# Kernel optimization log

Hardware: AMD Instinct MI355X
Metric: run time of the kernel (lower is better)

## Reference

```python
import jax, jax.numpy as jnp
import numpy as np

K = 3  # from init kwarg


def setup_inputs() -> dict:
    key = jax.random.key(0)
    k1, k2 = jax.random.split(key)
    B, N, D = 32, 2048, 128
    features = jax.random.normal(k1, (B, N, D), dtype=jnp.float32)
    strength = jax.random.uniform(k2, (), dtype=jnp.float32)
    return {"features": features, "strength": strength}


def reference(features, strength):
    B, N, D = features.shape
    k = min(K, N - 1)
    x = jax.lax.stop_gradient(features)  # torch uses features.detach() for the mix path

    # pairwise euclidean distance (torch.cdist, p=2): ||a||^2 + ||b||^2 - 2 a.b
    sq = jnp.sum(x * x, axis=-1)                     # (B, N)
    d2 = sq[:, :, None] + sq[:, None, :] - 2.0 * jnp.einsum('bnd,bmd->bnm', x, x)
    dist = jnp.sqrt(jnp.maximum(d2, 0.0))            # (B, N, N)

    # mask self-distance with +1e6 on the diagonal
    eye = jnp.eye(N, dtype=dist.dtype)
    dist = dist + eye[None, :, :] * 1000000.0

    # k smallest -> top_k of negated distances
    _, idx = jax.lax.top_k(-dist, k)                 # idx: (B, N, k)

    # gather neighbor features: gathered[b,n,j] = x[b, idx[b,n,j]]
    gathered = x[jnp.arange(B)[:, None, None], idx]  # (B, N, k, D)
    mix = jnp.mean(gathered, axis=2)                 # (B, N, D)

    s = jnp.clip(strength, 0.0, 1.0)
    return (1.0 - s) * features + s * mix
```

## Files before the change

kernel.cpp:

```cpp
#include <hip/hip_runtime.h>
#include <cfloat>

#define BB 32
#define NN 2048
#define DD 128
#define RM 128
#define CN 64

typedef __attribute__((ext_vector_type(8))) short short8;
typedef __attribute__((ext_vector_type(4))) float float4v;

__device__ __forceinline__ unsigned short f2bf(float f) {
    unsigned int u = __builtin_bit_cast(unsigned int, f);
    u += 0x7FFFu + ((u >> 16) & 1u);
    return (unsigned short)(u >> 16);
}

__device__ __forceinline__ unsigned int umn(unsigned int a, unsigned int b) { return a < b ? a : b; }
__device__ __forceinline__ unsigned int umx(unsigned int a, unsigned int b) { return a > b ? a : b; }
#define CSU(a, b) { unsigned int _lo = umn(a, b), _hi = umx(a, b); (a) = _lo; (b) = _hi; }

__device__ __forceinline__ void gl2lds16(const unsigned short* g, unsigned short* l) {
    __builtin_amdgcn_global_load_lds(
        (const __attribute__((address_space(1))) void*)g,
        (__attribute__((address_space(3))) void*)l, 16, 0, 0);
}

__global__ __launch_bounds__(256) void prep_kernel(const float* __restrict__ x,
        unsigned short* __restrict__ xb16, float* __restrict__ sq) {
    int t = blockIdx.x * 256 + threadIdx.x;
    int row = t >> 2;
    int q = t & 3;
    const float4* xp = reinterpret_cast<const float4*>(x + (size_t)row * DD + q * 32);
    unsigned short* op = xb16 + (size_t)row * DD + q * 32;
    float acc = 0.f;
#pragma unroll
    for (int i = 0; i < 4; ++i) {
        float4 v0 = xp[2 * i], v1 = xp[2 * i + 1];
        acc += v0.x * v0.x + v0.y * v0.y + v0.z * v0.z + v0.w * v0.w;
        acc += v1.x * v1.x + v1.y * v1.y + v1.z * v1.z + v1.w * v1.w;
        short8 pk;
        pk[0] = (short)f2bf(v0.x); pk[1] = (short)f2bf(v0.y);
        pk[2] = (short)f2bf(v0.z); pk[3] = (short)f2bf(v0.w);
        pk[4] = (short)f2bf(v1.x); pk[5] = (short)f2bf(v1.y);
        pk[6] = (short)f2bf(v1.z); pk[7] = (short)f2bf(v1.w);
        *reinterpret_cast<short8*>(op + i * 8) = pk;
    }
    acc += __shfl_xor(acc, 1);
    acc += __shfl_xor(acc, 2);
    if (q == 0) sq[row] = acc;
}

__global__ __launch_bounds__(256) void sq_kernel(const float* __restrict__ x,
                                                 float* __restrict__ sq) {
    int t = blockIdx.x * 256 + threadIdx.x;
    int row = t >> 2;
    int q = t & 3;
    const float4* xp = reinterpret_cast<const float4*>(x + (size_t)row * DD + q * 32);
    float acc = 0.f;
#pragma unroll
    for (int i = 0; i < 8; ++i) {
        float4 v = xp[i];
        acc += v.x * v.x + v.y * v.y + v.z * v.z + v.w * v.w;
    }
    acc += __shfl_xor(acc, 1);
    acc += __shfl_xor(acc, 2);
    if (q == 0) sq[row] = acc;
}

template<bool PRE>
__global__ __launch_bounds__(256, 2) void knn_kernel(const float* __restrict__ x,
        const unsigned short* __restrict__ xb16g,
        const float* __restrict__ sqv, const float* __restrict__ strength,
        float* __restrict__ out) {
    __shared__ __align__(16) unsigned short btile[2 * CN * DD];
    __shared__ unsigned int cand8[RM * 8];

    const int b = blockIdx.x;
    const int row0 = blockIdx.y * RM;
    const int tid = threadIdx.x;
    const int w = tid >> 6;
    const int lane = tid & 63;
    const int m = lane & 15;
    const int quad = lane >> 4;
    const float* __restrict__ xb = x + (size_t)b * NN * DD;
    const unsigned short* __restrict__ gb = PRE ? xb16g + (size_t)b * NN * DD : nullptr;

    short8 afrag[2][4];
    if constexpr (PRE) {
#pragma unroll
        for (int rg = 0; rg < 2; ++rg)
#pragma unroll
            for (int kc = 0; kc < 4; ++kc)
                afrag[rg][kc] = *reinterpret_cast<const short8*>(
                    gb + (size_t)(row0 + 32 * w + rg * 16 + m) * DD + kc * 32 + quad * 8);
    } else {
#pragma unroll
        for (int rg = 0; rg < 2; ++rg)
#pragma unroll
            for (int kc = 0; kc < 4; ++kc) {
                const float4* src = reinterpret_cast<const float4*>(
                    xb + (size_t)(row0 + 32 * w + rg * 16 + m) * DD + kc * 32 + quad * 8);
                float4 v0 = src[0], v1 = src[1];
                short8 pk;
                pk[0] = (short)f2bf(v0.x); pk[1] = (short)f2bf(v0.y);
                pk[2] = (short)f2bf(v0.z); pk[3] = (short)f2bf(v0.w);
                pk[4] = (short)f2bf(v1.x); pk[5] = (short)f2bf(v1.y);
                pk[6] = (short)f2bf(v1.z); pk[7] = (short)f2bf(v1.w);
                afrag[rg][kc] = pk;
            }
    }

    {
        unsigned short* buf = btile;
        if constexpr (PRE) {
#pragma unroll
            for (int l = 0; l < 4; ++l) {
                int f = (l * 4 + w) * 64 + lane;
                int r = f >> 4, p = f & 15;
                int c = p ^ (r & 7);
                gl2lds16(gb + (size_t)r * DD + c * 8, buf + (l * 4 + w) * 512);
            }
        } else {
#pragma unroll
            for (int l = 0; l < 4; ++l) {
                int id = l * 256 + tid;
                int r = id >> 4, c = id & 15, p = c ^ (r & 7);
                const float4* src = reinterpret_cast<const float4*>(xb + (size_t)r * DD + c * 8);
                float4 v0 = src[0], v1 = src[1];
                short8 pk;
                pk[0] = (short)f2bf(v0.x); pk[1] = (short)f2bf(v0.y);
                pk[2] = (short)f2bf(v0.z); pk[3] = (short)f2bf(v0.w);
                pk[4] = (short)f2bf(v1.x); pk[5] = (short)f2bf(v1.y);
                pk[6] = (short)f2bf(v1.z); pk[7] = (short)f2bf(v1.w);
                *reinterpret_cast<short8*>(buf + r * DD + p * 8) = pk;
            }
        }
    }
    __syncthreads();

    unsigned int tk[2][4][4];
#pragma unroll
    for (int rg = 0; rg < 2; ++rg)
#pragma unroll
        for (int i = 0; i < 4; ++i)
#pragma unroll
            for (int q = 0; q < 4; ++q) tk[rg][i][q] = 0xFFFFFFFFu;

    for (int ct = 0; ct < NN / CN; ++ct) {
        unsigned short* cur = btile + (size_t)(ct & 1) * CN * DD;
        unsigned short* nxt = btile + (size_t)((ct + 1) & 1) * CN * DD;

        if (ct + 1 < NN / CN) {
            int cb = (ct + 1) * CN;
            if constexpr (PRE) {
#pragma unroll
                for (int l = 0; l < 4; ++l) {
                    int f = (l * 4 + w) * 64 + lane;
                    int r = f >> 4, p = f & 15;
                    int c = p ^ (r & 7);
                    gl2lds16(gb + (size_t)(cb + r) * DD + c * 8, nxt + (l * 4 + w) * 512);
                }
            } else {
#pragma unroll
                for (int l = 0; l < 4; ++l) {
                    int id = l * 256 + tid;
                    int r = id >> 4, c = id & 15, p = c ^ (r & 7);
                    const float4* src = reinterpret_cast<const float4*>(xb + (size_t)(cb + r) * DD + c * 8);
                    float4 v0 = src[0], v1 = src[1];
                    short8 pk;
                    pk[0] = (short)f2bf(v0.x); pk[1] = (short)f2bf(v0.y);
                    pk[2] = (short)f2bf(v0.z); pk[3] = (short)f2bf(v0.w);
                    pk[4] = (short)f2bf(v1.x); pk[5] = (short)f2bf(v1.y);
                    pk[6] = (short)f2bf(v1.z); pk[7] = (short)f2bf(v1.w);
                    *reinterpret_cast<short8*>(nxt + r * DD + p * 8) = pk;
                }
            }
        }

        float sqb[4];
#pragma unroll
        for (int cc = 0; cc < 4; ++cc)
            sqb[cc] = sqv[(size_t)b * NN + ct * CN + cc * 16 + m] + 1024.0f;

        float4v acc[2][4];
#pragma unroll
        for (int rg = 0; rg < 2; ++rg)
#pragma unroll
            for (int cc = 0; cc < 4; ++cc) acc[rg][cc] = (float4v){0.f, 0.f, 0.f, 0.f};
#pragma unroll
        for (int kc = 0; kc < 4; ++kc) {
            short8 bfrag[4];
#pragma unroll
            for (int cc = 0; cc < 4; ++cc) {
                int rl = cc * 16 + m;
                int p = (kc * 4 + quad) ^ (m & 7);
                bfrag[cc] = *reinterpret_cast<const short8*>(cur + rl * DD + p * 8);
            }
#pragma unroll
            for (int rg = 0; rg < 2; ++rg)
#pragma unroll
                for (int cc = 0; cc < 4; ++cc)
                    acc[rg][cc] = __builtin_amdgcn_mfma_f32_16x16x32_bf16(
                        afrag[rg][kc], bfrag[cc], acc[rg][cc], 0, 0, 0);
        }

#pragma unroll
        for (int cc = 0; cc < 4; ++cc) {
            unsigned int col = (unsigned int)(ct * CN + cc * 16 + m);
#pragma unroll
            for (int rg = 0; rg < 2; ++rg)
#pragma unroll
                for (int reg = 0; reg < 4; ++reg) {
                    float scb = fmaf(-2.f, acc[rg][cc][reg], sqb[cc]);
                    unsigned int key = (__builtin_bit_cast(unsigned int, scb) & 0xFFFFF800u) | col;
                    unsigned int n;
                    n = umn(tk[rg][reg][0], key); key = umx(tk[rg][reg][0], key); tk[rg][reg][0] = n;
                    n = umn(tk[rg][reg][1], key); key = umx(tk[rg][reg][1], key); tk[rg][reg][1] = n;
                    n = umn(tk[rg][reg][2], key); key = umx(tk[rg][reg][2], key); tk[rg][reg][2] = n;
                    tk[rg][reg][3] = umn(tk[rg][reg][3], key);
                }
        }

        __syncthreads();
    }

#pragma unroll
    for (int rg = 0; rg < 2; ++rg)
#pragma unroll
        for (int reg = 0; reg < 4; ++reg) {
            unsigned int e[8];
#pragma unroll
            for (int j = 0; j < 4; ++j) e[j] = tk[rg][reg][j];
#pragma unroll
            for (int j = 4; j < 8; ++j) e[j] = 0xFFFFFFFFu;
#pragma unroll
            for (int st = 0; st < 4; ++st) {
                int mask = 1 << st;
                unsigned int rv[8];
#pragma unroll
                for (int j = 0; j < 8; ++j)
                    rv[j] = (unsigned int)__shfl_xor((int)e[7 - j], mask, 64);
#pragma unroll
                for (int j = 0; j < 8; ++j) e[j] = umn(e[j], rv[j]);
                CSU(e[0], e[4]); CSU(e[1], e[5]); CSU(e[2], e[6]); CSU(e[3], e[7]);
                CSU(e[0], e[2]); CSU(e[1], e[3]); CSU(e[4], e[6]); CSU(e[5], e[7]);
                CSU(e[0], e[1]); CSU(e[2], e[3]); CSU(e[4], e[5]); CSU(e[6], e[7]);
            }
            if (m == 0) {
                int row = 32 * w + rg * 16 + quad * 4 + reg;
#pragma unroll
                for (int j = 0; j < 8; ++j) cand8[row * 8 + j] = e[j];
            }
        }
    __syncthreads();

    double* refd = reinterpret_cast<double*>(btile);
    int* best3 = reinterpret_cast<int*>(btile) + 2048;

    {
        int r = tid >> 1, h = tid & 1;
        int grow = row0 + r;
        int ci[4];
#pragma unroll
        for (int j = 0; j < 4; ++j) ci[j] = (int)(cand8[r * 8 + h * 4 + j] & 0x7FFu);
        const float* pr = xb + (size_t)grow * DD;
        const float* pc[4];
#pragma unroll
        for (int j = 0; j < 4; ++j) pc[j] = xb + (size_t)ci[j] * DD;
        double a[4] = {0.0, 0.0, 0.0, 0.0};
#pragma unroll 4
        for (int d4 = 0; d4 < 32; ++d4) {
            float4 wv = *reinterpret_cast<const float4*>(pr + d4 * 4);
#pragma unroll
            for (int j = 0; j < 4; ++j) {
                float4 v = *reinterpret_cast<const float4*>(pc[j] + d4 * 4);
                double d;
                d = (double)wv.x - (double)v.x; a[j] += d * d;
                d = (double)wv.y - (double)v.y; a[j] += d * d;
                d = (double)wv.z - (double)v.z; a[j] += d * d;
                d = (double)wv.w - (double)v.w; a[j] += d * d;
            }
        }
#pragma unroll
        for (int j = 0; j < 4; ++j)
            refd[r * 8 + h * 4 + j] = (ci[j] == grow) ? DBL_MAX : a[j];
    }
    __syncthreads();

    if (tid < RM) {
        int r = tid;
        double b0 = DBL_MAX, b1 = DBL_MAX, b2 = DBL_MAX;
        int i0 = 0x7fffffff, i1 = 0x7fffffff, i2 = 0x7fffffff;
        for (int e = 0; e < 8; ++e) {
            double dv = refd[r * 8 + e];
            int ix = (int)(cand8[r * 8 + e] & 0x7FFu);
            if (dv < b2 || (dv == b2 && ix < i2)) {
                b2 = dv; i2 = ix;
                if (b1 > b2 || (b1 == b2 && i1 > i2)) { double td = b1; b1 = b2; b2 = td; int tn = i1; i1 = i2; i2 = tn; }
                if (b0 > b1 || (b0 == b1 && i0 > i1)) { double td = b0; b0 = b1; b1 = td; int tn = i0; i0 = i1; i1 = tn; }
            }
        }
        best3[r * 3 + 0] = i0; best3[r * 3 + 1] = i1; best3[r * 3 + 2] = i2;
    }
    __syncthreads();

    {
        int r = tid >> 1, q = tid & 1;
        float s = fminf(fmaxf(strength[0], 0.f), 1.f);
        const float* pa = xb + (size_t)(row0 + r) * DD + q * 64;
        const float* p1 = xb + (size_t)best3[r * 3 + 0] * DD + q * 64;
        const float* p2 = xb + (size_t)best3[r * 3 + 1] * DD + q * 64;
        const float* p3 = xb + (size_t)best3[r * 3 + 2] * DD + q * 64;
        float* po = out + ((size_t)b * NN + row0 + r) * DD + q * 64;
#pragma unroll
        for (int l = 0; l < 16; ++l) {
            float4 a  = *reinterpret_cast<const float4*>(pa + l * 4);
            float4 n1 = *reinterpret_cast<const float4*>(p1 + l * 4);
            float4 n2 = *reinterpret_cast<const float4*>(p2 + l * 4);
            float4 n3 = *reinterpret_cast<const float4*>(p3 + l * 4);
            float4 o;
            o.x = (1.f - s) * a.x + s * ((n1.x + n2.x + n3.x) / 3.f);
            o.y = (1.f - s) * a.y + s * ((n1.y + n2.y + n3.y) / 3.f);
            o.z = (1.f - s) * a.z + s * ((n1.z + n2.z + n3.z) / 3.f);
            o.w = (1.f - s) * a.w + s * ((n1.w + n2.w + n3.w) / 3.f);
            *reinterpret_cast<float4*>(po + l * 4) = o;
        }
    }
}

extern "C" void kernel_launch(void* const* d_in, const int* in_sizes, int n_in,
                              void* d_out, int out_size, void* d_ws, size_t ws_size,
                              hipStream_t stream) {
    const float* x = (const float*)d_in[0];
    const float* strength = (const float*)d_in[1];
    float* out = (float*)d_out;
    float* sq = (float*)d_ws;
    unsigned short* xb16 = (unsigned short*)((char*)d_ws + 256 * 1024);
    const size_t need = 256 * 1024 + (size_t)BB * NN * DD * sizeof(unsigned short);

    if (ws_size >= need) {
        prep_kernel<<<dim3((BB * NN * 4) / 256), 256, 0, stream>>>(x, xb16, sq);
        knn_kernel<true><<<dim3(BB, NN / RM), 256, 0, stream>>>(x, xb16, sq, strength, out);
    } else {
        sq_kernel<<<dim3((BB * NN * 4) / 256), 256, 0, stream>>>(x, sq);
        knn_kernel<false><<<dim3(BB, NN / RM), 256, 0, stream>>>(x, nullptr, sq, strength, out);
    }
}
```

Baseline: 200.8 us.

## Split kNN column range across blocks and move refinement into separate finish kernel

The main kNN kernel now splits the candidate column range into halves along a third grid dimension, doubling the block count. Each block writes its per-row top-8 approximate candidates to workspace. A new finish kernel recomputes exact double-precision distances for the merged candidates, picks the best three and performs the blend. The aim is more parallelism and occupancy (launch bounds raised to 4 blocks per CU) in exchange for an extra launch and a global round-trip of candidate keys. The last fallback path writes candidates without checking that the workspace is large enough.

```diff
diff --git a/kernel.cpp b/kernel.cpp
--- a/kernel.cpp
+++ b/kernel.cpp
@@ -69,15 +69,18 @@
 }
 
 template<bool PRE>
-__global__ __launch_bounds__(256, 2) void knn_kernel(const float* __restrict__ x,
+__global__ __launch_bounds__(256, 4) void knn_main(const float* __restrict__ x,
         const unsigned short* __restrict__ xb16g,
-        const float* __restrict__ sqv, const float* __restrict__ strength,
-        float* __restrict__ out) {
+        const float* __restrict__ sqv,
+        unsigned int* __restrict__ top8, int halves) {
     __shared__ __align__(16) unsigned short btile[2 * CN * DD];
-    __shared__ unsigned int cand8[RM * 8];
 
     const int b = blockIdx.x;
     const int row0 = blockIdx.y * RM;
+    const int h = blockIdx.z;
+    const int colspan = NN / halves;
+    const int col0 = h * colspan;
+    const int tiles = colspan / CN;
     const int tid = threadIdx.x;
     const int w = tid >> 6;
     const int lane = tid & 63;
@@ -119,14 +122,14 @@
                 int f = (l * 4 + w) * 64 + lane;
                 int r = f >> 4, p = f & 15;
                 int c = p ^ (r & 7);
-                gl2lds16(gb + (size_t)r * DD + c * 8, buf + (l * 4 + w) * 512);
+                gl2lds16(gb + (size_t)(col0 + r) * DD + c * 8, buf + (l * 4 + w) * 512);
             }
         } else {
 #pragma unroll
             for (int l = 0; l < 4; ++l) {
                 int id = l * 256 + tid;
                 int r = id >> 4, c = id & 15, p = c ^ (r & 7);
-                const float4* src = reinterpret_cast<const float4*>(xb + (size_t)r * DD + c * 8);
+                const float4* src = reinterpret_cast<const float4*>(xb + (size_t)(col0 + r) * DD + c * 8);
                 float4 v0 = src[0], v1 = src[1];
                 short8 pk;
                 pk[0] = (short)f2bf(v0.x); pk[1] = (short)f2bf(v0.y);
@@ -147,12 +150,13 @@
 #pragma unroll
             for (int q = 0; q < 4; ++q) tk[rg][i][q] = 0xFFFFFFFFu;
 
-    for (int ct = 0; ct < NN / CN; ++ct) {
+    for (int ct = 0; ct < tiles; ++ct) {
         unsigned short* cur = btile + (size_t)(ct & 1) * CN * DD;
         unsigned short* nxt = btile + (size_t)((ct + 1) & 1) * CN * DD;
-
-        if (ct + 1 < NN / CN) {
-            int cb = (ct + 1) * CN;
+        int colbase = col0 + ct * CN;
+
+        if (ct + 1 < tiles) {
+            int cb = colbase + CN;
             if constexpr (PRE) {
 #pragma unroll
                 for (int l = 0; l < 4; ++l) {
@@ -181,7 +185,7 @@
         float sqb[4];
 #pragma unroll
         for (int cc = 0; cc < 4; ++cc)
-            sqb[cc] = sqv[(size_t)b * NN + ct * CN + cc * 16 + m] + 1024.0f;
+            sqb[cc] = sqv[(size_t)b * NN + colbase + cc * 16 + m] + 1024.0f;
 
         float4v acc[2][4];
 #pragma unroll
@@ -207,7 +211,7 @@
 
 #pragma unroll
         for (int cc = 0; cc < 4; ++cc) {
-            unsigned int col = (unsigned int)(ct * CN + cc * 16 + m);
+            unsigned int col = (unsigned int)(colbase + cc * 16 + m);
 #pragma unroll
             for (int rg = 0; rg < 2; ++rg)
 #pragma unroll
@@ -248,73 +252,80 @@
                 CSU(e[0], e[1]); CSU(e[2], e[3]); CSU(e[4], e[5]); CSU(e[6], e[7]);
             }
             if (m == 0) {
-                int row = 32 * w + rg * 16 + quad * 4 + reg;
-#pragma unroll
-                for (int j = 0; j < 8; ++j) cand8[row * 8 + j] = e[j];
-            }
-        }
-    __syncthreads();
-
-    double* refd = reinterpret_cast<double*>(btile);
-    int* best3 = reinterpret_cast<int*>(btile) + 2048;
-
-    {
-        int r = tid >> 1, h = tid & 1;
-        int grow = row0 + r;
-        int ci[4];
-#pragma unroll
-        for (int j = 0; j < 4; ++j) ci[j] = (int)(cand8[r * 8 + h * 4 + j] & 0x7FFu);
-        const float* pr = xb + (size_t)grow * DD;
-        const float* pc[4];
-#pragma unroll
-        for (int j = 0; j < 4; ++j) pc[j] = xb + (size_t)ci[j] * DD;
-        double a[4] = {0.0, 0.0, 0.0, 0.0};
+                int row = row0 + 32 * w + rg * 16 + quad * 4 + reg;
+                unsigned int* dst = top8 + ((size_t)(b * NN + row) * halves + h) * 8;
+#pragma unroll
+                for (int j = 0; j < 8; ++j) dst[j] = e[j];
+            }
+        }
+}
+
+__global__ __launch_bounds__(256) void finish_kernel(const float* __restrict__ x,
+        const unsigned int* __restrict__ top8, const float* __restrict__ strength,
+        float* __restrict__ out, int halves) {
+    __shared__ double refd[32 * 16];
+    __shared__ int cidx[32 * 16];
+    __shared__ int best3[32 * 3];
+
+    const int tid = threadIdx.x;
+    const int r = tid >> 3;
+    const int t8 = tid & 7;
+    const int R = blockIdx.x * 32 + r;
+    const int b = R >> 11;
+    const int n = R & (NN - 1);
+    const float* __restrict__ xb = x + (size_t)b * NN * DD;
+    const int ncand = 8 * halves;
+
+    const unsigned int* keys = top8 + (size_t)R * ncand;
+    const int npt = halves;
+#pragma unroll 2
+    for (int t = 0; t < npt; ++t) {
+        int j = t8 * npt + t;
+        int ix = (int)(keys[j] & 0x7FFu);
+        const float* pc = xb + (size_t)ix * DD;
+        const float* pr = xb + (size_t)n * DD;
+        double a = 0.0;
 #pragma unroll 4
         for (int d4 = 0; d4 < 32; ++d4) {
             float4 wv = *reinterpret_cast<const float4*>(pr + d4 * 4);
-#pragma unroll
-            for (int j = 0; j < 4; ++j) {
-                float4 v = *reinterpret_cast<const float4*>(pc[j] + d4 * 4);
-                double d;
-                d = (double)wv.x - (double)v.x; a[j] += d * d;
-                d = (double)wv.y - (double)v.y; a[j] += d * d;
-                d = (double)wv.z - (double)v.z; a[j] += d * d;
-                d = (double)wv.w - (double)v.w; a[j] += d * d;
-            }
-        }
-#pragma unroll
-        for (int j = 0; j < 4; ++j)
-            refd[r * 8 + h * 4 + j] = (ci[j] == grow) ? DBL_MAX : a[j];
+            float4 v = *reinterpret_cast<const float4*>(pc + d4 * 4);
+            double d;
+            d = (double)wv.x - (double)v.x; a += d * d;
+            d = (double)wv.y - (double)v.y; a += d * d;
+            d = (double)wv.z - (double)v.z; a += d * d;
+            d = (double)wv.w - (double)v.w; a += d * d;
+        }
+        refd[r * 16 + j] = (ix == n) ? DBL_MAX : a;
+        cidx[r * 16 + j] = ix;
     }
     __syncthreads();
 
-    if (tid < RM) {
-        int r = tid;
+    if (tid < 32) {
+        int rr = tid;
         double b0 = DBL_MAX, b1 = DBL_MAX, b2 = DBL_MAX;
         int i0 = 0x7fffffff, i1 = 0x7fffffff, i2 = 0x7fffffff;
-        for (int e = 0; e < 8; ++e) {
-            double dv = refd[r * 8 + e];
-            int ix = (int)(cand8[r * 8 + e] & 0x7FFu);
+        for (int e = 0; e < ncand; ++e) {
+            double dv = refd[rr * 16 + e];
+            int ix = cidx[rr * 16 + e];
             if (dv < b2 || (dv == b2 && ix < i2)) {
                 b2 = dv; i2 = ix;
                 if (b1 > b2 || (b1 == b2 && i1 > i2)) { double td = b1; b1 = b2; b2 = td; int tn = i1; i1 = i2; i2 = tn; }
                 if (b0 > b1 || (b0 == b1 && i0 > i1)) { double td = b0; b0 = b1; b1 = td; int tn = i0; i0 = i1; i1 = tn; }
             }
         }
-        best3[r * 3 + 0] = i0; best3[r * 3 + 1] = i1; best3[r * 3 + 2] = i2;
+        best3[rr * 3 + 0] = i0; best3[rr * 3 + 1] = i1; best3[rr * 3 + 2] = i2;
     }
     __syncthreads();
 
     {
-        int r = tid >> 1, q = tid & 1;
         float s = fminf(fmaxf(strength[0], 0.f), 1.f);
-        const float* pa = xb + (size_t)(row0 + r) * DD + q * 64;
-        const float* p1 = xb + (size_t)best3[r * 3 + 0] * DD + q * 64;
-        const float* p2 = xb + (size_t)best3[r * 3 + 1] * DD + q * 64;
-        const float* p3 = xb + (size_t)best3[r * 3 + 2] * DD + q * 64;
-        float* po = out + ((size_t)b * NN + row0 + r) * DD + q * 64;
-#pragma unroll
-        for (int l = 0; l < 16; ++l) {
+        const float* pa = xb + (size_t)n * DD + t8 * 16;
+        const float* p1 = xb + (size_t)best3[r * 3 + 0] * DD + t8 * 16;
+        const float* p2 = xb + (size_t)best3[r * 3 + 1] * DD + t8 * 16;
+        const float* p3 = xb + (size_t)best3[r * 3 + 2] * DD + t8 * 16;
+        float* po = out + (size_t)R * DD + t8 * 16;
+#pragma unroll
+        for (int l = 0; l < 4; ++l) {
             float4 a  = *reinterpret_cast<const float4*>(pa + l * 4);
             float4 n1 = *reinterpret_cast<const float4*>(p1 + l * 4);
             float4 n2 = *reinterpret_cast<const float4*>(p2 + l * 4);
@@ -335,15 +346,36 @@
     const float* x = (const float*)d_in[0];
     const float* strength = (const float*)d_in[1];
     float* out = (float*)d_out;
+
+    const size_t SQ_B = 256 * 1024;
+    const size_t BF_B = (size_t)BB * NN * DD * 2;
     float* sq = (float*)d_ws;
-    unsigned short* xb16 = (unsigned short*)((char*)d_ws + 256 * 1024);
-    const size_t need = 256 * 1024 + (size_t)BB * NN * DD * sizeof(unsigned short);
-
-    if (ws_size >= need) {
+
+    const size_t need_pre2 = SQ_B + BF_B + (size_t)BB * NN * 2 * 8 * 4;
+    const size_t need_pre1 = SQ_B + BF_B + (size_t)BB * NN * 1 * 8 * 4;
+    const size_t need_raw2 = SQ_B + (size_t)BB * NN * 2 * 8 * 4;
+
+    if (ws_size >= need_pre2) {
+        unsigned short* xb16 = (unsigned short*)((char*)d_ws + SQ_B);
+        unsigned int* top8 = (unsigned int*)((char*)d_ws + SQ_B + BF_B);
         prep_kernel<<<dim3((BB * NN * 4) / 256), 256, 0, stream>>>(x, xb16, sq);
-        knn_kernel<true><<<dim3(BB, NN / RM), 256, 0, stream>>>(x, xb16, sq, strength, out);
+        knn_main<true><<<dim3(BB, NN / RM, 2), 256, 0, stream>>>(x, xb16, sq, top8, 2);
+        finish_kernel<<<dim3(BB * NN / 32), 256, 0, stream>>>(x, top8, strength, out, 2);
+    } else if (ws_size >= need_pre1) {
+        unsigned short* xb16 = (unsigned short*)((char*)d_ws + SQ_B);
+        unsigned int* top8 = (unsigned int*)((char*)d_ws + SQ_B + BF_B);
+        prep_kernel<<<dim3((BB * NN * 4) / 256), 256, 0, stream>>>(x, xb16, sq);
+        knn_main<true><<<dim3(BB, NN / RM, 1), 256, 0, stream>>>(x, xb16, sq, top8, 1);
+        finish_kernel<<<dim3(BB * NN / 32), 256, 0, stream>>>(x, top8, strength, out, 1);
+    } else if (ws_size >= need_raw2) {
+        unsigned int* top8 = (unsigned int*)((char*)d_ws + SQ_B);
+        sq_kernel<<<dim3((BB * NN * 4) / 256), 256, 0, stream>>>(x, sq);
+        knn_main<false><<<dim3(BB, NN / RM, 2), 256, 0, stream>>>(x, nullptr, sq, top8, 2);
+        finish_kernel<<<dim3(BB * NN / 32), 256, 0, stream>>>(x, top8, strength, out, 2);
     } else {
+        unsigned int* top8 = (unsigned int*)((char*)d_ws + SQ_B);
         sq_kernel<<<dim3((BB * NN * 4) / 256), 256, 0, stream>>>(x, sq);
-        knn_kernel<false><<<dim3(BB, NN / RM), 256, 0, stream>>>(x, nullptr, sq, strength, out);
-    }
-}
+        knn_main<false><<<dim3(BB, NN / RM, 1), 256, 0, stream>>>(x, nullptr, sq, top8, 1);
+        finish_kernel<<<dim3(BB * NN / 32), 256, 0, stream>>>(x, top8, strength, out, 1);
+    }
+}
```

After: 256.0 us. +27.5%, slower.
